# Optimization experiments

Hardware: AMD Instinct MI355X
Metric: run time of the kernel (lower is better)

The kernel has to match this reference:

```python
import jax, jax.numpy as jnp
import numpy as np

N, P, C, HID, H, W = 100000, 8, 256, 256, 512, 512
RADIUS = 2.0
D = C + 2


def setup_inputs() -> dict:
    key = jax.random.key(0)
    ks = jax.random.split(key, 9)
    return {
        "guided_queries": jax.random.normal(ks[0], (N, C), jnp.float32),
        "projection_coords": jax.random.uniform(ks[1], (N, 2), jnp.float32)
        * jnp.array([W - 1.0, H - 1.0], jnp.float32),
        "feature_map": jax.random.normal(ks[2], (H, W, C), jnp.float32),
        "off_ln_g": jnp.ones((D,), jnp.float32),
        "off_ln_b": jnp.zeros((D,), jnp.float32),
        "off_W1": jax.random.normal(ks[3], (D, HID), jnp.float32) * 0.05,
        "off_b1": jnp.zeros((HID,), jnp.float32),
        "off_W2": jax.random.normal(ks[4], (HID, HID), jnp.float32) * 0.05,
        "off_b2": jnp.zeros((HID,), jnp.float32),
        "off_W3": jax.random.normal(ks[5], (HID, P * 2), jnp.float32) * 0.01,
        "off_b3": jnp.zeros((P * 2,), jnp.float32),
        "wgt_ln_g": jnp.ones((D,), jnp.float32),
        "wgt_ln_b": jnp.zeros((D,), jnp.float32),
        "wgt_W1": jax.random.normal(ks[6], (D, HID), jnp.float32) * 0.05,
        "wgt_b1": jnp.zeros((HID,), jnp.float32),
        "wgt_W2": jax.random.normal(ks[7], (HID, HID), jnp.float32) * 0.05,
        "wgt_b2": jnp.zeros((HID,), jnp.float32),
        "wgt_W3": jax.random.normal(ks[8], (HID, P), jnp.float32) * 0.01,
        "wgt_b3": jnp.full((P,), 0.1, jnp.float32),
    }


def _layernorm(x, g, b, eps=1e-5):
    mu = x.mean(-1, keepdims=True)
    var = ((x - mu) ** 2).mean(-1, keepdims=True)
    return (x - mu) * jax.lax.rsqrt(var + eps) * g + b


def _mlp(x, W1, b1, W2, b2, W3, b3):
    # dropout is identity in eval mode
    h = jax.nn.relu(x @ W1 + b1)
    h = jax.nn.relu(h @ W2 + b2)
    return h @ W3 + b3


def _bilinear_border(fmap, coords):
    """fmap (H,W,C); coords (N,P,2) in pixel space -> (N,P,C).
    Matches F.grid_sample(mode='bilinear', padding_mode='border', align_corners=True)
    after the module's normalize + clamp(-1.1, 1.1)."""
    gx = jnp.clip(2.0 * coords[..., 0] / (W - 1) - 1.0, -1.1, 1.1)
    gy = jnp.clip(2.0 * coords[..., 1] / (H - 1) - 1.0, -1.1, 1.1)
    ix = jnp.clip((gx + 1.0) * 0.5 * (W - 1), 0.0, W - 1.0)  # border clamp
    iy = jnp.clip((gy + 1.0) * 0.5 * (H - 1), 0.0, H - 1.0)
    x0 = jnp.floor(ix)
    y0 = jnp.floor(iy)
    wx = (ix - x0)[..., None]
    wy = (iy - y0)[..., None]
    x0i = x0.astype(jnp.int32)
    y0i = y0.astype(jnp.int32)
    x1i = jnp.minimum(x0i + 1, W - 1)
    y1i = jnp.minimum(y0i + 1, H - 1)
    flat = fmap.reshape(H * W, C)
    v00 = flat[y0i * W + x0i]  # (N,P,C)
    v01 = flat[y0i * W + x1i]
    v10 = flat[y1i * W + x0i]
    v11 = flat[y1i * W + x1i]
    return (v00 * (1 - wx) + v01 * wx) * (1 - wy) + (v10 * (1 - wx) + v11 * wx) * wy


def reference(guided_queries, projection_coords, feature_map,
              off_ln_g, off_ln_b, off_W1, off_b1, off_W2, off_b2, off_W3, off_b3,
              wgt_ln_g, wgt_ln_b, wgt_W1, wgt_b1, wgt_W2, wgt_b2, wgt_W3, wgt_b3):
    x = jnp.concatenate([guided_queries, projection_coords], axis=-1)  # (N, C+2)
    off_raw = _mlp(_layernorm(x, off_ln_g, off_ln_b),
                   off_W1, off_b1, off_W2, off_b2, off_W3, off_b3)
    offsets = jnp.tanh(off_raw.reshape(-1, P, 2)) * RADIUS  # (N,P,2)
    wgt_raw = _mlp(_layernorm(x, wgt_ln_g, wgt_ln_b),
                   wgt_W1, wgt_b1, wgt_W2, wgt_b2, wgt_W3, wgt_b3)
    weights = jax.nn.softmax(wgt_raw, axis=-1)  # (N,P)
    coords = projection_coords[:, None, :] + offsets  # (N,P,2)
    sampled = _bilinear_border(feature_map, coords)  # (N,P,C)
    wsum = jnp.clip(weights.sum(-1, keepdims=True), 1e-8, None)
    nw = weights / wsum
    return jnp.sum(nw[..., None] * sampled, axis=1)  # (N,C)
```

## Files before the change

### kernel.cpp

```cpp
#include <hip/hip_runtime.h>

#define NQ   100000
#define PP   8
#define CC   256
#define HIDN 256
#define HH   512
#define WW   512
#define DD   258
#define KK1  288
#define KK2  256
#define TQ   16
#define XS_STRIDE 296
#define HA_STRIDE 264
#define HB_STRIDE 260

typedef __attribute__((ext_vector_type(8))) __bf16 bf16x8;
typedef __attribute__((ext_vector_type(4))) float  f32x4;

__device__ __forceinline__ unsigned short f2bf_hi(float v, float* rem) {
    __bf16 h = (__bf16)v;
    *rem = v - (float)h;
    return __builtin_bit_cast(unsigned short, h);
}
__device__ __forceinline__ unsigned short f2bf(float v) {
    __bf16 h = (__bf16)v;
    return __builtin_bit_cast(unsigned short, h);
}

#define WS_W1TH 0
#define WS_W1TL 294912
#define WS_W2TH 589824
#define WS_W2TL 851968
#define WS_W3T  1114112
#define WS_B1E  1138688

__global__ void prep_w1(const float* __restrict__ og, const float* __restrict__ obl,
                        const float* __restrict__ oW1, const float* __restrict__ ob1,
                        const float* __restrict__ wg, const float* __restrict__ wbl,
                        const float* __restrict__ wW1, const float* __restrict__ wb1,
                        unsigned short* __restrict__ w1th, unsigned short* __restrict__ w1tl,
                        float* __restrict__ b1e) {
    const int br = blockIdx.y, k = blockIdx.x, n = threadIdx.x;
    const float* g  = br ? wg  : og;
    const float* bl = br ? wbl : obl;
    const float* W1 = br ? wW1 : oW1;
    const float* b1 = br ? wb1 : ob1;
    float v = (k < DD) ? g[k] * W1[k * HIDN + n] : 0.f;
    float rem; unsigned short hi = f2bf_hi(v, &rem);
    size_t o = (size_t)br * 256 * KK1 + (size_t)n * KK1 + k;
    w1th[o] = hi; w1tl[o] = f2bf(rem);
    if (k == 0) {
        float s = b1[n];
        for (int kk = 0; kk < DD; ++kk) s += bl[kk] * W1[kk * HIDN + n];
        b1e[br * 256 + n] = s;
    }
}

__global__ void prep_w2(const float* __restrict__ oW2, const float* __restrict__ wW2,
                        unsigned short* __restrict__ w2th, unsigned short* __restrict__ w2tl) {
    const int br = blockIdx.y, k = blockIdx.x, n = threadIdx.x;
    const float* W2 = br ? wW2 : oW2;
    float v = W2[k * HIDN + n];
    float rem; unsigned short hi = f2bf_hi(v, &rem);
    size_t o = (size_t)br * 256 * KK2 + (size_t)n * KK2 + k;
    w2th[o] = hi; w2tl[o] = f2bf(rem);
}

__global__ void prep_w3(const float* __restrict__ oW3, const float* __restrict__ wW3,
                        float* __restrict__ w3t) {
    const int br = blockIdx.x, t = threadIdx.x;
    if (br == 0) {
        const int c = t & 15, kb = t >> 4;
        for (int i = 0; i < 16; ++i) { int k = kb * 16 + i; w3t[c * 256 + k] = oW3[k * 16 + c]; }
    } else {
        const int c = t & 7, kb = t >> 3;
        for (int i = 0; i < 8; ++i)  { int k = kb * 8 + i;  w3t[(16 + c) * 256 + k] = wW3[k * 8 + c]; }
    }
}

__launch_bounds__(256, 3)
__global__ void fused_kernel(const float* __restrict__ gq, const float* __restrict__ pc,
                             const float* __restrict__ fmap,
                             const unsigned short* __restrict__ w1th, const unsigned short* __restrict__ w1tl,
                             const unsigned short* __restrict__ w2th, const unsigned short* __restrict__ w2tl,
                             const float* __restrict__ w3t, const float* __restrict__ b1e,
                             const float* __restrict__ ob2, const float* __restrict__ ob3,
                             const float* __restrict__ wb2, const float* __restrict__ wb3,
                             float* __restrict__ out) {
    __shared__ __align__(16) unsigned short xsh[TQ * XS_STRIDE];
    __shared__ __align__(16) unsigned short xsl[TQ * XS_STRIDE];
    __shared__ __align__(16) unsigned short hah[TQ * HA_STRIDE];
    __shared__ __align__(16) unsigned short hal[TQ * HA_STRIDE];
    __shared__ __align__(16) float hb[TQ * HB_STRIDE];
    __shared__ __align__(16) float raw[TQ * 24];
    __shared__ __align__(16) float pcs[TQ * 2];

    const int t    = threadIdx.x;
    const int q0   = blockIdx.x * TQ;
    const int lane = t & 63;
    const int wv   = t >> 6;
    const int quad = lane >> 4;
    const int l15  = lane & 15;

    for (int i = t; i < TQ * XS_STRIDE / 2; i += 256) {
        ((unsigned int*)xsh)[i] = 0u; ((unsigned int*)xsl)[i] = 0u;
    }
    for (int q = 0; q < TQ; ++q)
        hb[q * HB_STRIDE + t] = gq[(size_t)(q0 + q) * CC + t];
    if (t < TQ * 2) {
        float v = pc[(size_t)q0 * 2 + t];
        pcs[t] = v;
        hb[(t >> 1) * HB_STRIDE + CC + (t & 1)] = v;
    }
    __syncthreads();

    for (int qi = 0; qi < TQ; qi += 4) {
        const int q = qi + wv;
        float s = 0.f, ss = 0.f;
        for (int k = lane; k < DD; k += 64) {
            float v = hb[q * HB_STRIDE + k]; s += v; ss += v * v;
        }
        for (int off = 32; off > 0; off >>= 1) {
            s += __shfl_xor(s, off, 64); ss += __shfl_xor(ss, off, 64);
        }
        const float mu = s * (1.f / DD);
        const float var = fmaxf(ss * (1.f / DD) - mu * mu, 0.f);
        const float rs = rsqrtf(var + 1e-5f);
        for (int k = lane; k < DD; k += 64) {
            float v = (hb[q * HB_STRIDE + k] - mu) * rs;
            float rem; xsh[q * XS_STRIDE + k] = f2bf_hi(v, &rem);
            xsl[q * XS_STRIDE + k] = f2bf(rem);
        }
    }
    __syncthreads();

    for (int br = 0; br < 2; ++br) {
        {
            f32x4 acc[4];
            #pragma unroll
            for (int nt = 0; nt < 4; ++nt) {
                float b = b1e[br * 256 + wv * 64 + nt * 16 + l15];
                acc[nt] = (f32x4){b, b, b, b};
            }
            const unsigned short* Wh = w1th + (size_t)br * 256 * KK1;
            const unsigned short* Wl = w1tl + (size_t)br * 256 * KK1;
            const unsigned short* axh = xsh + l15 * XS_STRIDE + quad * 8;
            const unsigned short* axl = xsl + l15 * XS_STRIDE + quad * 8;
            for (int k0 = 0; k0 < KK1; k0 += 32) {
                const bf16x8 ah = *(const bf16x8*)(axh + k0);
                const bf16x8 al = *(const bf16x8*)(axl + k0);
                #pragma unroll
                for (int nt = 0; nt < 4; ++nt) {
                    const size_t n = wv * 64 + nt * 16 + l15;
                    const bf16x8 bh = *(const bf16x8*)(Wh + n * KK1 + k0 + quad * 8);
                    const bf16x8 bl = *(const bf16x8*)(Wl + n * KK1 + k0 + quad * 8);
                    acc[nt] = __builtin_amdgcn_mfma_f32_16x16x32_bf16(ah, bh, acc[nt], 0, 0, 0);
                    acc[nt] = __builtin_amdgcn_mfma_f32_16x16x32_bf16(ah, bl, acc[nt], 0, 0, 0);
                    acc[nt] = __builtin_amdgcn_mfma_f32_16x16x32_bf16(al, bh, acc[nt], 0, 0, 0);
                }
            }
            #pragma unroll
            for (int nt = 0; nt < 4; ++nt) {
                const int n = wv * 64 + nt * 16 + l15;
                #pragma unroll
                for (int r = 0; r < 4; ++r) {
                    const int m = quad * 4 + r;
                    float v = fmaxf(acc[nt][r], 0.f);
                    float rem; hah[m * HA_STRIDE + n] = f2bf_hi(v, &rem);
                    hal[m * HA_STRIDE + n] = f2bf(rem);
                }
            }
        }
        __syncthreads();

        {
            const float* b2 = br ? wb2 : ob2;
            f32x4 acc[4];
            #pragma unroll
            for (int nt = 0; nt < 4; ++nt) {
                float b = b2[wv * 64 + nt * 16 + l15];
                acc[nt] = (f32x4){b, b, b, b};
            }
            const unsigned short* Wh = w2th + (size_t)br * 256 * KK2;
            const unsigned short* Wl = w2tl + (size_t)br * 256 * KK2;
            const unsigned short* axh = hah + l15 * HA_STRIDE + quad * 8;
            const unsigned short* axl = hal + l15 * HA_STRIDE + quad * 8;
            for (int k0 = 0; k0 < KK2; k0 += 32) {
                const bf16x8 ah = *(const bf16x8*)(axh + k0);
                const bf16x8 al = *(const bf16x8*)(axl + k0);
                #pragma unroll
                for (int nt = 0; nt < 4; ++nt) {
                    const size_t n = wv * 64 + nt * 16 + l15;
                    const bf16x8 bh = *(const bf16x8*)(Wh + n * KK2 + k0 + quad * 8);
                    const bf16x8 bl = *(const bf16x8*)(Wl + n * KK2 + k0 + quad * 8);
                    acc[nt] = __builtin_amdgcn_mfma_f32_16x16x32_bf16(ah, bh, acc[nt], 0, 0, 0);
                    acc[nt] = __builtin_amdgcn_mfma_f32_16x16x32_bf16(ah, bl, acc[nt], 0, 0, 0);
                    acc[nt] = __builtin_amdgcn_mfma_f32_16x16x32_bf16(al, bh, acc[nt], 0, 0, 0);
                }
            }
            #pragma unroll
            for (int nt = 0; nt < 4; ++nt) {
                const int n = wv * 64 + nt * 16 + l15;
                #pragma unroll
                for (int r = 0; r < 4; ++r) {
                    const int m = quad * 4 + r;
                    hb[m * HB_STRIDE + n] = fmaxf(acc[nt][r], 0.f);
                }
            }
        }
        __syncthreads();

        if (br == 0) {
            const int q = t >> 4, c = t & 15;
            float s = ob3[c];
            const float4* wv4 = (const float4*)(w3t + c * 256);
            const float4* hv4 = (const float4*)(hb + q * HB_STRIDE);
            for (int k4 = 0; k4 < 64; ++k4) {
                float4 h = hv4[k4], w = wv4[k4];
                s += h.x * w.x + h.y * w.y + h.z * w.z + h.w * w.w;
            }
            raw[q * 24 + c] = s;
        } else if (t < TQ * 8) {
            const int q = t >> 3, c = t & 7;
            float s = wb3[c];
            const float4* wv4 = (const float4*)(w3t + (16 + c) * 256);
            const float4* hv4 = (const float4*)(hb + q * HB_STRIDE);
            for (int k4 = 0; k4 < 64; ++k4) {
                float4 h = hv4[k4], w = wv4[k4];
                s += h.x * w.x + h.y * w.y + h.z * w.z + h.w * w.w;
            }
            raw[q * 24 + 16 + c] = s;
        }
        __syncthreads();
    }

    int*   sidx = (int*)xsh;
    float* sw   = (float*)xsl;
    if (t < TQ) {
        const int q = t;
        float m = -1e30f;
        #pragma unroll
        for (int p = 0; p < 8; ++p) m = fmaxf(m, raw[q * 24 + 16 + p]);
        float e[8]; float S = 0.f;
        #pragma unroll
        for (int p = 0; p < 8; ++p) { e[p] = expf(raw[q * 24 + 16 + p] - m); S += e[p]; }
        float s2 = 0.f;
        #pragma unroll
        for (int p = 0; p < 8; ++p) { e[p] /= S; s2 += e[p]; }
        const float inv = 1.f / fmaxf(s2, 1e-8f);

        const float px = pcs[q * 2 + 0], py = pcs[q * 2 + 1];
        #pragma unroll
        for (int p = 0; p < 8; ++p) {
            const float cx = px + 2.f * tanhf(raw[q * 24 + 2 * p]);
            const float cy = py + 2.f * tanhf(raw[q * 24 + 2 * p + 1]);
            const float gx = fminf(fmaxf(2.f * cx * (1.f / (WW - 1)) - 1.f, -1.1f), 1.1f);
            const float gy = fminf(fmaxf(2.f * cy * (1.f / (HH - 1)) - 1.f, -1.1f), 1.1f);
            const float ix = fminf(fmaxf((gx + 1.f) * 0.5f * (WW - 1), 0.f), (float)(WW - 1));
            const float iy = fminf(fmaxf((gy + 1.f) * 0.5f * (HH - 1), 0.f), (float)(HH - 1));
            const float x0 = floorf(ix), y0 = floorf(iy);
            const float wx = ix - x0, wy = iy - y0;
            const int x0i = (int)x0, y0i = (int)y0;
            const int x1i = min(x0i + 1, WW - 1), y1i = min(y0i + 1, HH - 1);
            const float nwp = e[p] * inv;
            const int b = (q * 8 + p) * 4;
            sidx[b + 0] = (y0i * WW + x0i) * (CC / 4);
            sidx[b + 1] = (y0i * WW + x1i) * (CC / 4);
            sidx[b + 2] = (y1i * WW + x0i) * (CC / 4);
            sidx[b + 3] = (y1i * WW + x1i) * (CC / 4);
            sw[b + 0] = (1.f - wx) * (1.f - wy) * nwp;
            sw[b + 1] = wx * (1.f - wy) * nwp;
            sw[b + 2] = (1.f - wx) * wy * nwp;
            sw[b + 3] = wx * wy * nwp;
        }
    }
    __syncthreads();

    const float4* fm4 = (const float4*)fmap;
    float4* out4 = (float4*)out;
    #pragma unroll
    for (int qq = 0; qq < 4; ++qq) {
        const int q = wv * 4 + qq;
        float4 acc; acc.x = acc.y = acc.z = acc.w = 0.f;
        for (int p = 0; p < 8; ++p) {
            const int b = (q * 8 + p) * 4;
            const int i00 = sidx[b + 0] + lane;
            const int i01 = sidx[b + 1] + lane;
            const int i10 = sidx[b + 2] + lane;
            const int i11 = sidx[b + 3] + lane;
            const float a00 = sw[b + 0], a01 = sw[b + 1], a10 = sw[b + 2], a11 = sw[b + 3];
            const float4 v00 = fm4[i00], v01 = fm4[i01], v10 = fm4[i10], v11 = fm4[i11];
            acc.x += a00 * v00.x + a01 * v01.x + a10 * v10.x + a11 * v11.x;
            acc.y += a00 * v00.y + a01 * v01.y + a10 * v10.y + a11 * v11.y;
            acc.z += a00 * v00.z + a01 * v01.z + a10 * v10.z + a11 * v11.z;
            acc.w += a00 * v00.w + a01 * v01.w + a10 * v10.w + a11 * v11.w;
        }
        out4[(size_t)(q0 + q) * (CC / 4) + lane] = acc;
    }
}

extern "C" void kernel_launch(void* const* d_in, const int* in_sizes, int n_in,
                              void* d_out, int out_size, void* d_ws, size_t ws_size,
                              hipStream_t stream) {
    const float* gq   = (const float*)d_in[0];
    const float* pc   = (const float*)d_in[1];
    const float* fmap = (const float*)d_in[2];
    const float* og   = (const float*)d_in[3];
    const float* obl  = (const float*)d_in[4];
    const float* oW1  = (const float*)d_in[5];
    const float* ob1  = (const float*)d_in[6];
    const float* oW2  = (const float*)d_in[7];
    const float* ob2  = (const float*)d_in[8];
    const float* oW3  = (const float*)d_in[9];
    const float* ob3  = (const float*)d_in[10];
    const float* wg   = (const float*)d_in[11];
    const float* wbl  = (const float*)d_in[12];
    const float* wW1  = (const float*)d_in[13];
    const float* wb1  = (const float*)d_in[14];
    const float* wW2  = (const float*)d_in[15];
    const float* wb2  = (const float*)d_in[16];
    const float* wW3  = (const float*)d_in[17];
    const float* wb3  = (const float*)d_in[18];

    char* ws = (char*)d_ws;
    unsigned short* w1th = (unsigned short*)(ws + WS_W1TH);
    unsigned short* w1tl = (unsigned short*)(ws + WS_W1TL);
    unsigned short* w2th = (unsigned short*)(ws + WS_W2TH);
    unsigned short* w2tl = (unsigned short*)(ws + WS_W2TL);
    float* w3t = (float*)(ws + WS_W3T);
    float* b1e = (float*)(ws + WS_B1E);
    float* out = (float*)d_out;

    prep_w1<<<dim3(KK1, 2), 256, 0, stream>>>(og, obl, oW1, ob1, wg, wbl, wW1, wb1, w1th, w1tl, b1e);
    prep_w2<<<dim3(KK2, 2), 256, 0, stream>>>(oW2, wW2, w2th, w2tl);
    prep_w3<<<2, 256, 0, stream>>>(oW3, wW3, w3t);
    fused_kernel<<<NQ / TQ, 256, 0, stream>>>(gq, pc, fmap, w1th, w1tl, w2th, w2tl, w3t, b1e,
                                              ob2, ob3, wb2, wb3, out);
}
```

Baseline: 1.464 ms.

## Double query tile to 32 with 512 threads, reuse one LDS buffer across layers

```diff
diff --git a/kernel.cpp b/kernel.cpp
--- a/kernel.cpp
+++ b/kernel.cpp
@@ -9,13 +9,14 @@
 #define DD   258
 #define KK1  288
 #define KK2  256
-#define TQ   16
+#define TQ   32
+#define NTHR 512
 #define XS_STRIDE 296
-#define HA_STRIDE 264
-#define HB_STRIDE 260
 
 typedef __attribute__((ext_vector_type(8))) __bf16 bf16x8;
 typedef __attribute__((ext_vector_type(4))) float  f32x4;
+typedef __attribute__((ext_vector_type(4))) unsigned short u16x4;
+typedef __attribute__((ext_vector_type(8))) unsigned short u16x8;
 
 __device__ __forceinline__ unsigned short f2bf_hi(float v, float* rem) {
     __bf16 h = (__bf16)v;
@@ -25,6 +26,10 @@
 __device__ __forceinline__ unsigned short f2bf(float v) {
     __bf16 h = (__bf16)v;
     return __builtin_bit_cast(unsigned short, h);
+}
+__device__ __forceinline__ float bf2f(unsigned short h) {
+    unsigned int u = ((unsigned int)h) << 16;
+    return __builtin_bit_cast(float, u);
 }
 
 #define WS_W1TH 0
@@ -78,7 +83,7 @@
     }
 }
 
-__launch_bounds__(256, 3)
+__launch_bounds__(NTHR, 4)
 __global__ void fused_kernel(const float* __restrict__ gq, const float* __restrict__ pc,
                              const float* __restrict__ fmap,
                              const unsigned short* __restrict__ w1th, const unsigned short* __restrict__ w1tl,
@@ -89,9 +94,6 @@
                              float* __restrict__ out) {
     __shared__ __align__(16) unsigned short xsh[TQ * XS_STRIDE];
     __shared__ __align__(16) unsigned short xsl[TQ * XS_STRIDE];
-    __shared__ __align__(16) unsigned short hah[TQ * HA_STRIDE];
-    __shared__ __align__(16) unsigned short hal[TQ * HA_STRIDE];
-    __shared__ __align__(16) float hb[TQ * HB_STRIDE];
     __shared__ __align__(16) float raw[TQ * 24];
     __shared__ __align__(16) float pcs[TQ * 2];
 
@@ -102,132 +104,185 @@
     const int quad = lane >> 4;
     const int l15  = lane & 15;
 
-    for (int i = t; i < TQ * XS_STRIDE / 2; i += 256) {
+    for (int i = t; i < TQ * XS_STRIDE / 2; i += NTHR) {
         ((unsigned int*)xsh)[i] = 0u; ((unsigned int*)xsl)[i] = 0u;
     }
-    for (int q = 0; q < TQ; ++q)
-        hb[q * HB_STRIDE + t] = gq[(size_t)(q0 + q) * CC + t];
-    if (t < TQ * 2) {
-        float v = pc[(size_t)q0 * 2 + t];
-        pcs[t] = v;
-        hb[(t >> 1) * HB_STRIDE + CC + (t & 1)] = v;
-    }
+    if (t < TQ * 2) pcs[t] = pc[(size_t)q0 * 2 + t];
     __syncthreads();
 
-    for (int qi = 0; qi < TQ; qi += 4) {
-        const int q = qi + wv;
-        float s = 0.f, ss = 0.f;
-        for (int k = lane; k < DD; k += 64) {
-            float v = hb[q * HB_STRIDE + k]; s += v; ss += v * v;
-        }
-        for (int off = 32; off > 0; off >>= 1) {
-            s += __shfl_xor(s, off, 64); ss += __shfl_xor(ss, off, 64);
-        }
-        const float mu = s * (1.f / DD);
-        const float var = fmaxf(ss * (1.f / DD) - mu * mu, 0.f);
-        const float rs = rsqrtf(var + 1e-5f);
-        for (int k = lane; k < DD; k += 64) {
-            float v = (hb[q * HB_STRIDE + k] - mu) * rs;
-            float rem; xsh[q * XS_STRIDE + k] = f2bf_hi(v, &rem);
-            xsl[q * XS_STRIDE + k] = f2bf(rem);
-        }
-    }
-    __syncthreads();
+    const float4* gq4 = (const float4*)gq;
 
     for (int br = 0; br < 2; ++br) {
+        #pragma unroll
+        for (int qq = 0; qq < 4; ++qq) {
+            const int q = wv * 4 + qq;
+            const float4 v = gq4[(size_t)(q0 + q) * 64 + lane];
+            const float px = pcs[q * 2 + 0], py = pcs[q * 2 + 1];
+            float s  = v.x + v.y + v.z + v.w;
+            float ss = v.x * v.x + v.y * v.y + v.z * v.z + v.w * v.w;
+            if (lane == 0) { s += px + py; ss += px * px + py * py; }
+            #pragma unroll
+            for (int off = 32; off > 0; off >>= 1) {
+                s += __shfl_xor(s, off, 64); ss += __shfl_xor(ss, off, 64);
+            }
+            const float mu = s * (1.f / DD);
+            const float var = fmaxf(ss * (1.f / DD) - mu * mu, 0.f);
+            const float rs = rsqrtf(var + 1e-5f);
+            const float n0 = (v.x - mu) * rs, n1 = (v.y - mu) * rs;
+            const float n2 = (v.z - mu) * rs, n3 = (v.w - mu) * rs;
+            float r0, r1, r2, r3;
+            u16x4 hh; u16x4 ll;
+            hh[0] = f2bf_hi(n0, &r0); hh[1] = f2bf_hi(n1, &r1);
+            hh[2] = f2bf_hi(n2, &r2); hh[3] = f2bf_hi(n3, &r3);
+            ll[0] = f2bf(r0); ll[1] = f2bf(r1); ll[2] = f2bf(r2); ll[3] = f2bf(r3);
+            *(u16x4*)(&xsh[q * XS_STRIDE + lane * 4]) = hh;
+            *(u16x4*)(&xsl[q * XS_STRIDE + lane * 4]) = ll;
+            if (lane == 0) {
+                const float nx = (px - mu) * rs, ny = (py - mu) * rs;
+                float rx, ry;
+                xsh[q * XS_STRIDE + 256] = f2bf_hi(nx, &rx);
+                xsh[q * XS_STRIDE + 257] = f2bf_hi(ny, &ry);
+                xsl[q * XS_STRIDE + 256] = f2bf(rx);
+                xsl[q * XS_STRIDE + 257] = f2bf(ry);
+            }
+        }
+        __syncthreads();
+
         {
-            f32x4 acc[4];
-            #pragma unroll
-            for (int nt = 0; nt < 4; ++nt) {
-                float b = b1e[br * 256 + wv * 64 + nt * 16 + l15];
-                acc[nt] = (f32x4){b, b, b, b};
-            }
+            f32x4 acc[2][2];
+            #pragma unroll
+            for (int mt = 0; mt < 2; ++mt)
+                #pragma unroll
+                for (int nt = 0; nt < 2; ++nt) {
+                    float b = b1e[br * 256 + wv * 32 + nt * 16 + l15];
+                    acc[mt][nt] = (f32x4){b, b, b, b};
+                }
             const unsigned short* Wh = w1th + (size_t)br * 256 * KK1;
             const unsigned short* Wl = w1tl + (size_t)br * 256 * KK1;
-            const unsigned short* axh = xsh + l15 * XS_STRIDE + quad * 8;
-            const unsigned short* axl = xsl + l15 * XS_STRIDE + quad * 8;
+            const unsigned short* a0h = xsh + l15 * XS_STRIDE + quad * 8;
+            const unsigned short* a0l = xsl + l15 * XS_STRIDE + quad * 8;
+            const unsigned short* a1h = a0h + 16 * XS_STRIDE;
+            const unsigned short* a1l = a0l + 16 * XS_STRIDE;
             for (int k0 = 0; k0 < KK1; k0 += 32) {
-                const bf16x8 ah = *(const bf16x8*)(axh + k0);
-                const bf16x8 al = *(const bf16x8*)(axl + k0);
-                #pragma unroll
-                for (int nt = 0; nt < 4; ++nt) {
-                    const size_t n = wv * 64 + nt * 16 + l15;
+                const bf16x8 ah0 = *(const bf16x8*)(a0h + k0);
+                const bf16x8 al0 = *(const bf16x8*)(a0l + k0);
+                const bf16x8 ah1 = *(const bf16x8*)(a1h + k0);
+                const bf16x8 al1 = *(const bf16x8*)(a1l + k0);
+                #pragma unroll
+                for (int nt = 0; nt < 2; ++nt) {
+                    const size_t n = wv * 32 + nt * 16 + l15;
                     const bf16x8 bh = *(const bf16x8*)(Wh + n * KK1 + k0 + quad * 8);
                     const bf16x8 bl = *(const bf16x8*)(Wl + n * KK1 + k0 + quad * 8);
-                    acc[nt] = __builtin_amdgcn_mfma_f32_16x16x32_bf16(ah, bh, acc[nt], 0, 0, 0);
-                    acc[nt] = __builtin_amdgcn_mfma_f32_16x16x32_bf16(ah, bl, acc[nt], 0, 0, 0);
-                    acc[nt] = __builtin_amdgcn_mfma_f32_16x16x32_bf16(al, bh, acc[nt], 0, 0, 0);
-                }
-            }
-            #pragma unroll
-            for (int nt = 0; nt < 4; ++nt) {
-                const int n = wv * 64 + nt * 16 + l15;
-                #pragma unroll
-                for (int r = 0; r < 4; ++r) {
-                    const int m = quad * 4 + r;
-                    float v = fmaxf(acc[nt][r], 0.f);
-                    float rem; hah[m * HA_STRIDE + n] = f2bf_hi(v, &rem);
-                    hal[m * HA_STRIDE + n] = f2bf(rem);
-                }
-            }
+                    acc[0][nt] = __builtin_amdgcn_mfma_f32_16x16x32_bf16(ah0, bh, acc[0][nt], 0, 0, 0);
+                    acc[0][nt] = __builtin_amdgcn_mfma_f32_16x16x32_bf16(ah0, bl, acc[0][nt], 0, 0, 0);
+                    acc[0][nt] = __builtin_amdgcn_mfma_f32_16x16x32_bf16(al0, bh, acc[0][nt], 0, 0, 0);
+                    acc[1][nt] = __builtin_amdgcn_mfma_f32_16x16x32_bf16(ah1, bh, acc[1][nt], 0, 0, 0);
+                    acc[1][nt] = __builtin_amdgcn_mfma_f32_16x16x32_bf16(ah1, bl, acc[1][nt], 0, 0, 0);
+                    acc[1][nt] = __builtin_amdgcn_mfma_f32_16x16x32_bf16(al1, bh, acc[1][nt], 0, 0, 0);
+                }
+            }
+            __syncthreads();
+            #pragma unroll
+            for (int mt = 0; mt < 2; ++mt)
+                #pragma unroll
+                for (int nt = 0; nt < 2; ++nt) {
+                    const int n = wv * 32 + nt * 16 + l15;
+                    #pragma unroll
+                    for (int r = 0; r < 4; ++r) {
+                        const int m = mt * 16 + quad * 4 + r;
+                        float v = fmaxf(acc[mt][nt][r], 0.f);
+                        float rem;
+                        xsh[m * XS_STRIDE + n] = f2bf_hi(v, &rem);
+                        xsl[m * XS_STRIDE + n] = f2bf(rem);
+                    }
+                }
         }
         __syncthreads();
 
         {
             const float* b2 = br ? wb2 : ob2;
-            f32x4 acc[4];
-            #pragma unroll
-            for (int nt = 0; nt < 4; ++nt) {
-                float b = b2[wv * 64 + nt * 16 + l15];
-                acc[nt] = (f32x4){b, b, b, b};
-            }
+            f32x4 acc[2][2];
+            #pragma unroll
+            for (int mt = 0; mt < 2; ++mt)
+                #pragma unroll
+                for (int nt = 0; nt < 2; ++nt) {
+                    float b = b2[wv * 32 + nt * 16 + l15];
+                    acc[mt][nt] = (f32x4){b, b, b, b};
+                }
             const unsigned short* Wh = w2th + (size_t)br * 256 * KK2;
             const unsigned short* Wl = w2tl + (size_t)br * 256 * KK2;
-            const unsigned short* axh = hah + l15 * HA_STRIDE + quad * 8;
-            const unsigned short* axl = hal + l15 * HA_STRIDE + quad * 8;
+            const unsigned short* a0h = xsh + l15 * XS_STRIDE + quad * 8;
+            const unsigned short* a0l = xsl + l15 * XS_STRIDE + quad * 8;
+            const unsigned short* a1h = a0h + 16 * XS_STRIDE;
+            const unsigned short* a1l = a0l + 16 * XS_STRIDE;
             for (int k0 = 0; k0 < KK2; k0 += 32) {
-                const bf16x8 ah = *(const bf16x8*)(axh + k0);
-                const bf16x8 al = *(const bf16x8*)(axl + k0);
-                #pragma unroll
-                for (int nt = 0; nt < 4; ++nt) {
-                    const size_t n = wv * 64 + nt * 16 + l15;
+                const bf16x8 ah0 = *(const bf16x8*)(a0h + k0);
+                const bf16x8 al0 = *(const bf16x8*)(a0l + k0);
+                const bf16x8 ah1 = *(const bf16x8*)(a1h + k0);
+                const bf16x8 al1 = *(const bf16x8*)(a1l + k0);
+                #pragma unroll
+                for (int nt = 0; nt < 2; ++nt) {
+                    const size_t n = wv * 32 + nt * 16 + l15;
                     const bf16x8 bh = *(const bf16x8*)(Wh + n * KK2 + k0 + quad * 8);
                     const bf16x8 bl = *(const bf16x8*)(Wl + n * KK2 + k0 + quad * 8);
-                    acc[nt] = __builtin_amdgcn_mfma_f32_16x16x32_bf16(ah, bh, acc[nt], 0, 0, 0);
-                    acc[nt] = __builtin_amdgcn_mfma_f32_16x16x32_bf16(ah, bl, acc[nt], 0, 0, 0);
-                    acc[nt] = __builtin_amdgcn_mfma_f32_16x16x32_bf16(al, bh, acc[nt], 0, 0, 0);
-                }
-            }
-            #pragma unroll
-            for (int nt = 0; nt < 4; ++nt) {
-                const int n = wv * 64 + nt * 16 + l15;
-                #pragma unroll
-                for (int r = 0; r < 4; ++r) {
-                    const int m = quad * 4 + r;
-                    hb[m * HB_STRIDE + n] = fmaxf(acc[nt][r], 0.f);
-                }
-            }
+                    acc[0][nt] = __builtin_amdgcn_mfma_f32_16x16x32_bf16(ah0, bh, acc[0][nt], 0, 0, 0);
+                    acc[0][nt] = __builtin_amdgcn_mfma_f32_16x16x32_bf16(ah0, bl, acc[0][nt], 0, 0, 0);
+                    acc[0][nt] = __builtin_amdgcn_mfma_f32_16x16x32_bf16(al0, bh, acc[0][nt], 0, 0, 0);
+                    acc[1][nt] = __builtin_amdgcn_mfma_f32_16x16x32_bf16(ah1, bh, acc[1][nt], 0, 0, 0);
+                    acc[1][nt] = __builtin_amdgcn_mfma_f32_16x16x32_bf16(ah1, bl, acc[1][nt], 0, 0, 0);
+                    acc[1][nt] = __builtin_amdgcn_mfma_f32_16x16x32_bf16(al1, bh, acc[1][nt], 0, 0, 0);
+                }
+            }
+            __syncthreads();
+            #pragma unroll
+            for (int mt = 0; mt < 2; ++mt)
+                #pragma unroll
+                for (int nt = 0; nt < 2; ++nt) {
+                    const int n = wv * 32 + nt * 16 + l15;
+                    #pragma unroll
+                    for (int r = 0; r < 4; ++r) {
+                        const int m = mt * 16 + quad * 4 + r;
+                        float v = fmaxf(acc[mt][nt][r], 0.f);
+                        float rem;
+                        xsh[m * XS_STRIDE + n] = f2bf_hi(v, &rem);
+                        xsl[m * XS_STRIDE + n] = f2bf(rem);
+                    }
+                }
         }
         __syncthreads();
 
         if (br == 0) {
             const int q = t >> 4, c = t & 15;
             float s = ob3[c];
-            const float4* wv4 = (const float4*)(w3t + c * 256);
-            const float4* hv4 = (const float4*)(hb + q * HB_STRIDE);
-            for (int k4 = 0; k4 < 64; ++k4) {
-                float4 h = hv4[k4], w = wv4[k4];
-                s += h.x * w.x + h.y * w.y + h.z * w.z + h.w * w.w;
+            const float4* w4 = (const float4*)(w3t + c * 256);
+            const unsigned short* hrow = xsh + q * XS_STRIDE;
+            const unsigned short* lrow = xsl + q * XS_STRIDE;
+            for (int k = 0; k < 256; k += 8) {
+                const u16x8 hi = *(const u16x8*)(hrow + k);
+                const u16x8 lo = *(const u16x8*)(lrow + k);
+                const float4 wa = w4[(k >> 2)];
+                const float4 wb = w4[(k >> 2) + 1];
+                s += (bf2f(hi[0]) + bf2f(lo[0])) * wa.x + (bf2f(hi[1]) + bf2f(lo[1])) * wa.y
+                   + (bf2f(hi[2]) + bf2f(lo[2])) * wa.z + (bf2f(hi[3]) + bf2f(lo[3])) * wa.w
+                   + (bf2f(hi[4]) + bf2f(lo[4])) * wb.x + (bf2f(hi[5]) + bf2f(lo[5])) * wb.y
+                   + (bf2f(hi[6]) + bf2f(lo[6])) * wb.z + (bf2f(hi[7]) + bf2f(lo[7])) * wb.w;
             }
             raw[q * 24 + c] = s;
         } else if (t < TQ * 8) {
             const int q = t >> 3, c = t & 7;
             float s = wb3[c];
-            const float4* wv4 = (const float4*)(w3t + (16 + c) * 256);
-            const float4* hv4 = (const float4*)(hb + q * HB_STRIDE);
-            for (int k4 = 0; k4 < 64; ++k4) {
-                float4 h = hv4[k4], w = wv4[k4];
-                s += h.x * w.x + h.y * w.y + h.z * w.z + h.w * w.w;
+            const float4* w4 = (const float4*)(w3t + (16 + c) * 256);
+            const unsigned short* hrow = xsh + q * XS_STRIDE;
+            const unsigned short* lrow = xsl + q * XS_STRIDE;
+            for (int k = 0; k < 256; k += 8) {
+                const u16x8 hi = *(const u16x8*)(hrow + k);
+                const u16x8 lo = *(const u16x8*)(lrow + k);
+                const float4 wa = w4[(k >> 2)];
+                const float4 wb = w4[(k >> 2) + 1];
+                s += (bf2f(hi[0]) + bf2f(lo[0])) * wa.x + (bf2f(hi[1]) + bf2f(lo[1])) * wa.y
+                   + (bf2f(hi[2]) + bf2f(lo[2])) * wa.z + (bf2f(hi[3]) + bf2f(lo[3])) * wa.w
+                   + (bf2f(hi[4]) + bf2f(lo[4])) * wb.x + (bf2f(hi[5]) + bf2f(lo[5])) * wb.y
+                   + (bf2f(hi[6]) + bf2f(lo[6])) * wb.z + (bf2f(hi[7]) + bf2f(lo[7])) * wb.w;
             }
             raw[q * 24 + 16 + c] = s;
         }
@@ -334,6 +389,6 @@
     prep_w1<<<dim3(KK1, 2), 256, 0, stream>>>(og, obl, oW1, ob1, wg, wbl, wW1, wb1, w1th, w1tl, b1e);
     prep_w2<<<dim3(KK2, 2), 256, 0, stream>>>(oW2, wW2, w2th, w2tl);
     prep_w3<<<2, 256, 0, stream>>>(oW3, wW3, w3t);
-    fused_kernel<<<NQ / TQ, 256, 0, stream>>>(gq, pc, fmap, w1th, w1tl, w2th, w2tl, w3t, b1e,
-                                              ob2, ob3, wb2, wb3, out);
-}
+    fused_kernel<<<NQ / TQ, NTHR, 0, stream>>>(gq, pc, fmap, w1th, w1tl, w2th, w2tl, w3t, b1e,
+                                               ob2, ob3, wb2, wb3, out);
+}
```

Result: faster. 1.197 ms (-18.2%).
